# Kernel tuning notes

Hardware: AMD Instinct MI355X
Metric: run time of the kernel (lower is better)

The kernel has to match this reference:

```python
import jax, jax.numpy as jnp
import numpy as np

GS = 96  # grid_size per axis
NV, H_IM, W_IM = 8, 256, 256


def _world_grid():
    xs = jnp.linspace(-1.0, 1.0, GS)
    ys = jnp.linspace(-1.0, 1.0, GS)
    zs = jnp.linspace(0.0, 1.0, GS)
    gx, gy, gz = jnp.meshgrid(xs, ys, zs, indexing='ij')
    return jnp.stack([gx, gy, gz], -1).reshape(-1, 3)  # (N,3)


def _grid_sample(feats, grid):
    # feats (NV,C,H,W), grid (NV,P,2) normalized coords; bilinear,
    # align_corners=True, padding_mode='zeros' (matches F.grid_sample).
    n, C, H, W = feats.shape
    ix = (grid[..., 0] + 1.0) * (W - 1) * 0.5
    iy = (grid[..., 1] + 1.0) * (H - 1) * 0.5
    x0 = jnp.floor(ix); y0 = jnp.floor(iy)
    wx = (ix - x0)[..., None]; wy = (iy - y0)[..., None]
    x0i = x0.astype(jnp.int32); y0i = y0.astype(jnp.int32)
    b = jnp.arange(n)[:, None]
    def corner(yi, xi):
        valid = ((yi >= 0) & (yi < H) & (xi >= 0) & (xi < W)).astype(feats.dtype)
        v = feats[b, :, jnp.clip(yi, 0, H - 1), jnp.clip(xi, 0, W - 1)]  # (NV,P,C)
        return v * valid[..., None]
    v00 = corner(y0i, x0i); v01 = corner(y0i, x0i + 1)
    v10 = corner(y0i + 1, x0i); v11 = corner(y0i + 1, x0i + 1)
    return (v00 * (1 - wx) * (1 - wy) + v01 * wx * (1 - wy)
            + v10 * (1 - wx) * wy + v11 * wx * wy)


def _mlp_agg(x, w1, b1, w2, b2):
    h = jax.nn.relu(x @ w1.T + b1)
    return h @ w2.T + b2


def _forward(images, poses, focal, c, dw1, db1, dw2, db2, dw3, db3,
             ayz_w1, ayz_b1, ayz_w2, ayz_b2,
             axz_w1, axz_b1, axz_w2, axz_b2,
             axy_w1, axy_b1, axy_w2, axy_b2):
    nv, _, H, W = images.shape
    H_feat, W_feat = H // 2, W // 2
    stride = H / H_feat
    f = focal[0, 0] / stride
    f2 = jnp.stack([f, -f])                # y-focal flipped as in torch code
    c2 = c[0] / stride
    # features = unprocess_images(images): inverse of Normalize(0.5, 0.5)
    feats = images * 0.5 + 0.5             # (NV,3,H,W)

    wg = _world_grid()                     # (N,3)
    t = poses[:, :3, 3]; R = poses[:, :3, :3]
    d = wg[None] - t[:, None]              # (NV,N,3) dirs from cam center
    cam = jnp.einsum('npj,nji->npi', d, R) # world2camera: R^T (w - t)
    dnorm = jnp.linalg.norm(d + 1e-9, axis=-1)
    dirs = d / dnorm[..., None]

    uv = cam[..., :2] / cam[..., 2:3] * f2 + c2
    gxn = 2.0 * uv[..., 0] / (W_feat - 1) - 1.0
    gyn = 2.0 * uv[..., 1] / (H_feat - 1) - 1.0
    grid = jnp.stack([gxn, gyn], -1)       # (NV,N,2)
    mask_z = cam[..., 2] < 0.001
    inside = (jnp.abs(gxn) <= 1.0) & (jnp.abs(gyn) <= 1.0) & mask_z

    lat = _grid_sample(feats, grid) * inside[..., None].astype(images.dtype)  # (NV,N,3)
    out_latent = jnp.transpose(lat, (0, 2, 1))  # (NV,3,N)
    dirs = dirs * mask_z[..., None].astype(images.dtype)

    x = jnp.concatenate([lat, cam, dirs], -1)   # (NV,N,9)
    h = jax.nn.relu(x @ dw1.T + db1)
    h = jax.nn.relu(h @ dw2.T + db2)
    h = h @ dw3.T + db3                         # (NV,N,3)
    lat5 = h.reshape(1, nv, GS, GS, GS, 3)      # out_latent_2
    latm = lat5.mean(1)                         # (1,GS,GS,GS,3)

    coords = wg.reshape(1, GS, GS, GS, 3)
    w_yz = jax.nn.softmax(_mlp_agg(jnp.concatenate([latm, coords[..., 0:1]], -1), ayz_w1, ayz_b1, ayz_w2, ayz_b2), axis=1)
    w_xz = jax.nn.softmax(_mlp_agg(jnp.concatenate([latm, coords[..., 1:2]], -1), axz_w1, axz_b1, axz_w2, axz_b2), axis=2)
    w_xy = jax.nn.softmax(_mlp_agg(jnp.concatenate([latm, coords[..., 2:3]], -1), axy_w1, axy_b1, axy_w2, axy_b2), axis=3)

    fl_yz = (latm * w_yz).sum(1)   # (1,GS,GS,3)
    fl_xz = (latm * w_xz).sum(2)
    fl_xy = (latm * w_xy).sum(3)
    scene_xz = jnp.transpose(fl_xz, (0, 3, 1, 2))
    scene_xy = jnp.transpose(fl_xy, (0, 3, 1, 2))
    scene_yz = jnp.transpose(fl_yz, (0, 3, 1, 2))
    return scene_xz, scene_xy, scene_yz, out_latent, lat5


def _look_at(eye, target, up):
    f = target - eye; f = f / np.linalg.norm(f)
    z = -f
    x = np.cross(up, z); x = x / np.linalg.norm(x)
    y = np.cross(z, x)
    pose = np.eye(4, dtype=np.float32)
    pose[:3, 0] = x; pose[:3, 1] = y; pose[:3, 2] = z; pose[:3, 3] = eye
    return pose


def setup_inputs() -> dict:
    key = jax.random.key(0)
    ks = jax.random.split(key, 16)
    images = jax.random.normal(ks[0], (NV, 3, H_IM, W_IM), dtype=jnp.float32)
    # camera-to-world poses: ring of cameras looking at grid center (0,0,0.5)
    target = np.array([0.0, 0.0, 0.5], dtype=np.float32)
    up = np.array([0.0, 0.0, 1.0], dtype=np.float32)
    poses = np.stack([_look_at(np.array([3.0 * np.cos(a), 3.0 * np.sin(a), 1.5], dtype=np.float32), target, up)
                      for a in np.linspace(0, 2 * np.pi, NV, endpoint=False)])
    poses = jnp.asarray(poses)
    focal = jnp.full((1, 1), 300.0, dtype=jnp.float32)
    c = jnp.array([[W_IM / 2.0, H_IM / 2.0]], dtype=jnp.float32)

    def kaiming(k, shape):  # (out,in)
        return jax.random.normal(k, shape, dtype=jnp.float32) * np.sqrt(2.0 / shape[1])
    def bias(k, n):
        return jax.random.uniform(k, (n,), minval=-0.001, maxval=0.001, dtype=jnp.float32)

    inp = dict(images=images, poses=poses, focal=focal, c=c,
               dw1=kaiming(ks[1], (3, 9)), db1=bias(ks[2], 3),
               dw2=kaiming(ks[3], (3, 3)), db2=bias(ks[4], 3),
               dw3=kaiming(ks[5], (3, 3)), db3=bias(ks[6], 3),
               ayz_w1=kaiming(ks[7], (3, 4)), ayz_b1=bias(ks[8], 3),
               ayz_w2=kaiming(ks[9], (1, 3)), ayz_b2=bias(ks[10], 1),
               axz_w1=kaiming(ks[11], (3, 4)), axz_b1=bias(ks[12], 3),
               axz_w2=kaiming(ks[13], (1, 3)), axz_b2=bias(ks[14], 1),
               axy_w1=kaiming(ks[15], (3, 4)), axy_b1=bias(jax.random.fold_in(key, 99), 3),
               axy_w2=kaiming(jax.random.fold_in(key, 100), (1, 3)), axy_b2=bias(jax.random.fold_in(key, 101), 1))
    return inp


def reference(images, poses, focal, c, dw1, db1, dw2, db2, dw3, db3,
              ayz_w1, ayz_b1, ayz_w2, ayz_b2,
              axz_w1, axz_b1, axz_w2, axz_b2,
              axy_w1, axy_b1, axy_w2, axy_b2):
    return _forward(images, poses, focal, c, dw1, db1, dw2, db2, dw3, db3,
                    ayz_w1, ayz_b1, ayz_w2, ayz_b2,
                    axz_w1, axz_b1, axz_w2, axz_b2,
                    axy_w1, axy_b1, axy_w2, axy_b2)
```

## Files before the change

### kernel.cpp

```cpp
#include <hip/hip_runtime.h>
#include <math.h>

#define GSZ  96
#define GS2  (GSZ*GSZ)
#define NPTS (GSZ*GSZ*GSZ)
#define NVIEW 8
#define HIM  256
#define WIM  256

#define SCENE_SZ   (3*GS2)
#define OUTLAT_OFF (3*SCENE_SZ)
#define LAT5_OFF   (OUTLAT_OFF + NVIEW*3*NPTS)

__device__ __forceinline__ float red_max64(float v) {
    #pragma unroll
    for (int m = 32; m >= 1; m >>= 1) v = fmaxf(v, __shfl_xor(v, m, 64));
    return v;
}
__device__ __forceinline__ float red_sum64(float v) {
    #pragma unroll
    for (int m = 32; m >= 1; m >>= 1) v += __shfl_xor(v, m, 64);
    return v;
}

__global__ __launch_bounds__(256)
void k1_sample_mlp(const float* __restrict__ images, const float* __restrict__ poses,
                   const float* __restrict__ focal, const float* __restrict__ cc,
                   const float* __restrict__ dw1, const float* __restrict__ db1,
                   const float* __restrict__ dw2, const float* __restrict__ db2,
                   const float* __restrict__ dw3, const float* __restrict__ db3,
                   float* __restrict__ out_latent, float* __restrict__ lat5,
                   float* __restrict__ latm, int write_latm)
{
    const int p   = blockIdx.x * 256 + threadIdx.x;
    const int ix  = p / GS2;
    const int rem = p - ix * GS2;
    const int iy  = rem / GSZ;
    const int iz  = rem - iy * GSZ;
    const float wxv = (float)ix * (2.0f/95.0f) - 1.0f;
    const float wyv = (float)iy * (2.0f/95.0f) - 1.0f;
    const float wzv = (float)iz * (1.0f/95.0f);

    const float f   = focal[0] * 0.5f;
    const float c2x = cc[0] * 0.5f;
    const float c2y = cc[1] * 0.5f;

    float a0 = 0.f, a1 = 0.f, a2 = 0.f;

    for (int n = 0; n < NVIEW; ++n) {
        const float* ps = poses + n * 16;
        const float r00 = ps[0], r01 = ps[1], r02 = ps[2],  tx = ps[3];
        const float r10 = ps[4], r11 = ps[5], r12 = ps[6],  ty = ps[7];
        const float r20 = ps[8], r21 = ps[9], r22 = ps[10], tz = ps[11];

        const float dx = wxv - tx, dy = wyv - ty, dz = wzv - tz;
        const float camx = dx*r00 + dy*r10 + dz*r20;
        const float camy = dx*r01 + dy*r11 + dz*r21;
        const float camz = dx*r02 + dy*r12 + dz*r22;

        const float ex = dx + 1e-9f, ey = dy + 1e-9f, ez = dz + 1e-9f;
        const float dn = sqrtf(ex*ex + ey*ey + ez*ez);
        const bool  mz = camz < 0.001f;
        float d0 = 0.f, d1 = 0.f, d2 = 0.f;
        if (mz) { d0 = dx/dn; d1 = dy/dn; d2 = dz/dn; }

        const float u = camx/camz * f    + c2x;
        const float v = camy/camz * (-f) + c2y;
        const float gxn = 2.0f*u/127.0f - 1.0f;
        const float gyn = 2.0f*v/127.0f - 1.0f;

        float l0 = 0.f, l1 = 0.f, l2 = 0.f;
        const bool inside = (fabsf(gxn) <= 1.0f) && (fabsf(gyn) <= 1.0f) && mz;
        if (inside) {
            const float sx = (gxn + 1.0f) * 255.0f * 0.5f;
            const float sy = (gyn + 1.0f) * 255.0f * 0.5f;
            const float x0f = floorf(sx), y0f = floorf(sy);
            const float fx = sx - x0f, fy = sy - y0f;
            const int x0 = (int)x0f, y0 = (int)y0f;
            const int x1 = x0 + 1,  y1 = y0 + 1;
            const float vx0 = (x0 >= 0 && x0 < WIM) ? 1.f : 0.f;
            const float vx1 = (x1 >= 0 && x1 < WIM) ? 1.f : 0.f;
            const float vy0 = (y0 >= 0 && y0 < HIM) ? 1.f : 0.f;
            const float vy1 = (y1 >= 0 && y1 < HIM) ? 1.f : 0.f;
            const int cx0 = min(max(x0, 0), WIM-1), cx1 = min(max(x1, 0), WIM-1);
            const int cy0 = min(max(y0, 0), HIM-1), cy1 = min(max(y1, 0), HIM-1);
            const float w00 = (1.0f-fx)*(1.0f-fy)*vx0*vy0;
            const float w01 = fx*(1.0f-fy)*vx1*vy0;
            const float w10 = (1.0f-fx)*fy*vx0*vy1;
            const float w11 = fx*fy*vx1*vy1;
            const float* img = images + (size_t)n*3*HIM*WIM;
            #pragma unroll
            for (int ch = 0; ch < 3; ++ch) {
                const float* b = img + ch*HIM*WIM;
                const float p00 = b[cy0*WIM + cx0]*0.5f + 0.5f;
                const float p01 = b[cy0*WIM + cx1]*0.5f + 0.5f;
                const float p10 = b[cy1*WIM + cx0]*0.5f + 0.5f;
                const float p11 = b[cy1*WIM + cx1]*0.5f + 0.5f;
                const float lv  = p00*w00 + p01*w01 + p10*w10 + p11*w11;
                if (ch == 0) l0 = lv; else if (ch == 1) l1 = lv; else l2 = lv;
            }
        }

        __builtin_nontemporal_store(l0, out_latent + (size_t)n*3*NPTS + 0*NPTS + p);
        __builtin_nontemporal_store(l1, out_latent + (size_t)n*3*NPTS + 1*NPTS + p);
        __builtin_nontemporal_store(l2, out_latent + (size_t)n*3*NPTS + 2*NPTS + p);

        float xin[9] = {l0, l1, l2, camx, camy, camz, d0, d1, d2};
        float h1[3], h2[3], h3[3];
        #pragma unroll
        for (int k = 0; k < 3; ++k) {
            float s = 0.f;
            #pragma unroll
            for (int j = 0; j < 9; ++j) s += xin[j] * dw1[k*9 + j];
            s += db1[k];
            h1[k] = fmaxf(s, 0.f);
        }
        #pragma unroll
        for (int k = 0; k < 3; ++k) {
            float s = 0.f;
            #pragma unroll
            for (int j = 0; j < 3; ++j) s += h1[j] * dw2[k*3 + j];
            s += db2[k];
            h2[k] = fmaxf(s, 0.f);
        }
        #pragma unroll
        for (int k = 0; k < 3; ++k) {
            float s = 0.f;
            #pragma unroll
            for (int j = 0; j < 3; ++j) s += h2[j] * dw3[k*3 + j];
            s += db3[k];
            h3[k] = s;
        }

        float* lp = lat5 + ((size_t)n*NPTS + p)*3;
        __builtin_nontemporal_store(h3[0], lp + 0);
        __builtin_nontemporal_store(h3[1], lp + 1);
        __builtin_nontemporal_store(h3[2], lp + 2);
        a0 += h3[0]; a1 += h3[1]; a2 += h3[2];
    }

    if (write_latm) {
        latm[0*NPTS + p] = a0 * 0.125f;
        latm[1*NPTS + p] = a1 * 0.125f;
        latm[2*NPTS + p] = a2 * 0.125f;
    }
}

__global__ __launch_bounds__(64)
void k2_agg(const float* __restrict__ latm, const float* __restrict__ lat5, int use_ws,
            const float* __restrict__ yzw1, const float* __restrict__ yzb1,
            const float* __restrict__ yzw2, const float* __restrict__ yzb2,
            const float* __restrict__ xzw1, const float* __restrict__ xzb1,
            const float* __restrict__ xzw2, const float* __restrict__ xzb2,
            const float* __restrict__ xyw1, const float* __restrict__ xyb1,
            const float* __restrict__ xyw2, const float* __restrict__ xyb2,
            float* __restrict__ out)
{
    const int dir = blockIdx.y;
    const int l   = blockIdx.x;
    const int t   = threadIdx.x;
    const int la  = l / GSZ;
    const int lb  = l - la * GSZ;

    const float* w1 = (dir == 0) ? yzw1 : (dir == 1) ? xzw1 : xyw1;
    const float* b1 = (dir == 0) ? yzb1 : (dir == 1) ? xzb1 : xyb1;
    const float* w2 = (dir == 0) ? yzw2 : (dir == 1) ? xzw2 : xyw2;
    const float* b2 = (dir == 0) ? yzb2 : (dir == 1) ? xzb2 : xyb2;

    auto eval = [&](int vi, float& s, float& v0, float& v1, float& v2) {
        int p;
        float coord;
        if (dir == 0)      { p = vi*GS2 + la*GSZ + lb; coord = (float)vi*(2.0f/95.0f) - 1.0f; }
        else if (dir == 1) { p = la*GS2 + vi*GSZ + lb; coord = (float)vi*(2.0f/95.0f) - 1.0f; }
        else               { p = la*GS2 + lb*GSZ + vi; coord = (float)vi*(1.0f/95.0f); }
        if (use_ws) {
            v0 = latm[p]; v1 = latm[NPTS + p]; v2 = latm[2*NPTS + p];
        } else {
            v0 = 0.f; v1 = 0.f; v2 = 0.f;
            for (int n = 0; n < NVIEW; ++n) {
                const float* q = lat5 + ((size_t)n*NPTS + p)*3;
                v0 += q[0]; v1 += q[1]; v2 += q[2];
            }
            v0 *= 0.125f; v1 *= 0.125f; v2 *= 0.125f;
        }
        float h[3];
        #pragma unroll
        for (int k = 0; k < 3; ++k) {
            float a = v0*w1[k*4+0] + v1*w1[k*4+1] + v2*w1[k*4+2] + coord*w1[k*4+3] + b1[k];
            h[k] = fmaxf(a, 0.f);
        }
        s = h[0]*w2[0] + h[1]*w2[1] + h[2]*w2[2] + b2[0];
    };

    float s0, va0, va1, va2;
    eval(t, s0, va0, va1, va2);
    const bool hasB = (t < GSZ - 64);
    float s1 = -__builtin_inff(), vb0 = 0.f, vb1 = 0.f, vb2 = 0.f;
    if (hasB) eval(t + 64, s1, vb0, vb1, vb2);

    float m = red_max64(fmaxf(s0, s1));
    const float e0 = expf(s0 - m);
    const float e1 = hasB ? expf(s1 - m) : 0.f;

    float den = red_sum64(e0 + e1);
    float n0  = red_sum64(e0*va0 + e1*vb0);
    float n1  = red_sum64(e0*va1 + e1*vb1);
    float n2  = red_sum64(e0*va2 + e1*vb2);

    if (t == 0) {
        float* base = out + ((dir == 0) ? 2*SCENE_SZ : (dir == 1) ? 0 : SCENE_SZ);
        base[0*GS2 + la*GSZ + lb] = n0 / den;
        base[1*GS2 + la*GSZ + lb] = n1 / den;
        base[2*GS2 + la*GSZ + lb] = n2 / den;
    }
}

extern "C" void kernel_launch(void* const* d_in, const int* in_sizes, int n_in,
                              void* d_out, int out_size, void* d_ws, size_t ws_size,
                              hipStream_t stream) {
    const float* images = (const float*)d_in[0];
    const float* poses  = (const float*)d_in[1];
    const float* focal  = (const float*)d_in[2];
    const float* cc     = (const float*)d_in[3];
    const float* dw1 = (const float*)d_in[4];  const float* db1 = (const float*)d_in[5];
    const float* dw2 = (const float*)d_in[6];  const float* db2 = (const float*)d_in[7];
    const float* dw3 = (const float*)d_in[8];  const float* db3 = (const float*)d_in[9];
    const float* yzw1 = (const float*)d_in[10]; const float* yzb1 = (const float*)d_in[11];
    const float* yzw2 = (const float*)d_in[12]; const float* yzb2 = (const float*)d_in[13];
    const float* xzw1 = (const float*)d_in[14]; const float* xzb1 = (const float*)d_in[15];
    const float* xzw2 = (const float*)d_in[16]; const float* xzb2 = (const float*)d_in[17];
    const float* xyw1 = (const float*)d_in[18]; const float* xyb1 = (const float*)d_in[19];
    const float* xyw2 = (const float*)d_in[20]; const float* xyb2 = (const float*)d_in[21];

    float* out        = (float*)d_out;
    float* out_latent = out + OUTLAT_OFF;
    float* lat5       = out + LAT5_OFF;
    float* latm       = (float*)d_ws;
    const int use_ws  = (d_ws != nullptr &&
                         ws_size >= (size_t)NPTS * 3 * sizeof(float)) ? 1 : 0;

    hipLaunchKernelGGL(k1_sample_mlp, dim3(NPTS/256), dim3(256), 0, stream,
                       images, poses, focal, cc, dw1, db1, dw2, db2, dw3, db3,
                       out_latent, lat5, latm, use_ws);
    hipLaunchKernelGGL(k2_agg, dim3(GS2, 3), dim3(64), 0, stream,
                       latm, lat5, use_ws,
                       yzw1, yzb1, yzw2, yzb2,
                       xzw1, xzb1, xzw2, xzb2,
                       xyw1, xyb1, xyw2, xyb2,
                       out);
}
```

Measured before the change: 386.0 us.

## Interleave image channels, tile sampling in 2D, split aggregation into per-axis kernels

Adds a pre-pass that packs the three normalized image channels into float4 texels, so each bilinear corner becomes one vector load instead of three scattered loads. The sampling kernel now maps each block to a 16x16 y-z tile on one x slice, aiming for better locality of image gathers. Aggregation along x and y becomes one thread per line with an online softmax that reads coalesced across threads and keeps the weights in registers. Aggregation along z keeps the wave reduction but packs four lines per block. The cost is an extra kernel launch and an 8 MB workspace buffer for the packed images.

Result: faster. 308.8 us (-20.0%).

```diff
diff --git a/kernel.cpp b/kernel.cpp
--- a/kernel.cpp
+++ b/kernel.cpp
@@ -7,10 +7,14 @@
 #define NVIEW 8
 #define HIM  256
 #define WIM  256
+#define NPIX (HIM*WIM)
 
 #define SCENE_SZ   (3*GS2)
 #define OUTLAT_OFF (3*SCENE_SZ)
 #define LAT5_OFF   (OUTLAT_OFF + NVIEW*3*NPTS)
+
+#define LATM_BYTES ((size_t)3*NPTS*sizeof(float))
+#define IMG4_BYTES ((size_t)NVIEW*NPIX*sizeof(float4))
 
 __device__ __forceinline__ float red_max64(float v) {
     #pragma unroll
@@ -24,7 +28,24 @@
 }
 
 __global__ __launch_bounds__(256)
-void k1_sample_mlp(const float* __restrict__ images, const float* __restrict__ poses,
+void k0_interleave(const float* __restrict__ images, float4* __restrict__ img4)
+{
+    const int g   = blockIdx.x * 256 + threadIdx.x;
+    const int n   = g >> 16;
+    const int pix = g & (NPIX - 1);
+    const float* base = images + (size_t)n * 3 * NPIX + pix;
+    float4 v;
+    v.x = base[0]        * 0.5f + 0.5f;
+    v.y = base[NPIX]     * 0.5f + 0.5f;
+    v.z = base[2*NPIX]   * 0.5f + 0.5f;
+    v.w = 0.f;
+    img4[g] = v;
+}
+
+__global__ __launch_bounds__(256)
+void k1_sample_mlp(const float* __restrict__ images, const float4* __restrict__ img4,
+                   int use_img4,
+                   const float* __restrict__ poses,
                    const float* __restrict__ focal, const float* __restrict__ cc,
                    const float* __restrict__ dw1, const float* __restrict__ db1,
                    const float* __restrict__ dw2, const float* __restrict__ db2,
@@ -32,11 +53,13 @@
                    float* __restrict__ out_latent, float* __restrict__ lat5,
                    float* __restrict__ latm, int write_latm)
 {
-    const int p   = blockIdx.x * 256 + threadIdx.x;
-    const int ix  = p / GS2;
-    const int rem = p - ix * GS2;
-    const int iy  = rem / GSZ;
-    const int iz  = rem - iy * GSZ;
+    const int ty = threadIdx.x >> 4;
+    const int tz = threadIdx.x & 15;
+    const int iy = blockIdx.x * 16 + ty;
+    const int iz = blockIdx.y * 16 + tz;
+    const int ix = blockIdx.z;
+    const int p  = ix * GS2 + iy * GSZ + iz;
+
     const float wxv = (float)ix * (2.0f/95.0f) - 1.0f;
     const float wyv = (float)iy * (2.0f/95.0f) - 1.0f;
     const float wzv = (float)iz * (1.0f/95.0f);
@@ -50,10 +73,10 @@
     for (int n = 0; n < NVIEW; ++n) {
         const float* ps = poses + n * 16;
         const float r00 = ps[0], r01 = ps[1], r02 = ps[2],  tx = ps[3];
-        const float r10 = ps[4], r11 = ps[5], r12 = ps[6],  ty = ps[7];
-        const float r20 = ps[8], r21 = ps[9], r22 = ps[10], tz = ps[11];
-
-        const float dx = wxv - tx, dy = wyv - ty, dz = wzv - tz;
+        const float r10 = ps[4], r11 = ps[5], r12 = ps[6],  tyy = ps[7];
+        const float r20 = ps[8], r21 = ps[9], r22 = ps[10], tzz = ps[11];
+
+        const float dx = wxv - tx, dy = wyv - tyy, dz = wzv - tzz;
         const float camx = dx*r00 + dy*r10 + dz*r20;
         const float camy = dx*r01 + dy*r11 + dz*r21;
         const float camz = dx*r02 + dy*r12 + dz*r22;
@@ -88,16 +111,27 @@
             const float w01 = fx*(1.0f-fy)*vx1*vy0;
             const float w10 = (1.0f-fx)*fy*vx0*vy1;
             const float w11 = fx*fy*vx1*vy1;
-            const float* img = images + (size_t)n*3*HIM*WIM;
-            #pragma unroll
-            for (int ch = 0; ch < 3; ++ch) {
-                const float* b = img + ch*HIM*WIM;
-                const float p00 = b[cy0*WIM + cx0]*0.5f + 0.5f;
-                const float p01 = b[cy0*WIM + cx1]*0.5f + 0.5f;
-                const float p10 = b[cy1*WIM + cx0]*0.5f + 0.5f;
-                const float p11 = b[cy1*WIM + cx1]*0.5f + 0.5f;
-                const float lv  = p00*w00 + p01*w01 + p10*w10 + p11*w11;
-                if (ch == 0) l0 = lv; else if (ch == 1) l1 = lv; else l2 = lv;
+            if (use_img4) {
+                const float4* iv = img4 + (size_t)n * NPIX;
+                const float4 q00 = iv[cy0*WIM + cx0];
+                const float4 q01 = iv[cy0*WIM + cx1];
+                const float4 q10 = iv[cy1*WIM + cx0];
+                const float4 q11 = iv[cy1*WIM + cx1];
+                l0 = q00.x*w00 + q01.x*w01 + q10.x*w10 + q11.x*w11;
+                l1 = q00.y*w00 + q01.y*w01 + q10.y*w10 + q11.y*w11;
+                l2 = q00.z*w00 + q01.z*w01 + q10.z*w10 + q11.z*w11;
+            } else {
+                const float* img = images + (size_t)n*3*NPIX;
+                #pragma unroll
+                for (int ch = 0; ch < 3; ++ch) {
+                    const float* b = img + ch*NPIX;
+                    const float p00 = b[cy0*WIM + cx0]*0.5f + 0.5f;
+                    const float p01 = b[cy0*WIM + cx1]*0.5f + 0.5f;
+                    const float p10 = b[cy1*WIM + cx0]*0.5f + 0.5f;
+                    const float p11 = b[cy1*WIM + cx1]*0.5f + 0.5f;
+                    const float lv  = p00*w00 + p01*w01 + p10*w10 + p11*w11;
+                    if (ch == 0) l0 = lv; else if (ch == 1) l1 = lv; else l2 = lv;
+                }
             }
         }
 
@@ -112,24 +146,21 @@
             float s = 0.f;
             #pragma unroll
             for (int j = 0; j < 9; ++j) s += xin[j] * dw1[k*9 + j];
-            s += db1[k];
-            h1[k] = fmaxf(s, 0.f);
+            h1[k] = fmaxf(s + db1[k], 0.f);
         }
         #pragma unroll
         for (int k = 0; k < 3; ++k) {
             float s = 0.f;
             #pragma unroll
             for (int j = 0; j < 3; ++j) s += h1[j] * dw2[k*3 + j];
-            s += db2[k];
-            h2[k] = fmaxf(s, 0.f);
+            h2[k] = fmaxf(s + db2[k], 0.f);
         }
         #pragma unroll
         for (int k = 0; k < 3; ++k) {
             float s = 0.f;
             #pragma unroll
             for (int j = 0; j < 3; ++j) s += h2[j] * dw3[k*3 + j];
-            s += db3[k];
-            h3[k] = s;
+            h3[k] = s + db3[k];
         }
 
         float* lp = lat5 + ((size_t)n*NPTS + p)*3;
@@ -146,33 +177,35 @@
     }
 }
 
-__global__ __launch_bounds__(64)
-void k2_agg(const float* __restrict__ latm, const float* __restrict__ lat5, int use_ws,
-            const float* __restrict__ yzw1, const float* __restrict__ yzb1,
-            const float* __restrict__ yzw2, const float* __restrict__ yzb2,
-            const float* __restrict__ xzw1, const float* __restrict__ xzb1,
-            const float* __restrict__ xzw2, const float* __restrict__ xzb2,
-            const float* __restrict__ xyw1, const float* __restrict__ xyb1,
-            const float* __restrict__ xyw2, const float* __restrict__ xyb2,
-            float* __restrict__ out)
+__global__ __launch_bounds__(256)
+void k2a_lines(const float* __restrict__ latm, const float* __restrict__ lat5, int use_ws,
+               const float* __restrict__ yzw1, const float* __restrict__ yzb1,
+               const float* __restrict__ yzw2, const float* __restrict__ yzb2,
+               const float* __restrict__ xzw1, const float* __restrict__ xzb1,
+               const float* __restrict__ xzw2, const float* __restrict__ xzb2,
+               float* __restrict__ out)
 {
     const int dir = blockIdx.y;
-    const int l   = blockIdx.x;
-    const int t   = threadIdx.x;
-    const int la  = l / GSZ;
-    const int lb  = l - la * GSZ;
-
-    const float* w1 = (dir == 0) ? yzw1 : (dir == 1) ? xzw1 : xyw1;
-    const float* b1 = (dir == 0) ? yzb1 : (dir == 1) ? xzb1 : xyb1;
-    const float* w2 = (dir == 0) ? yzw2 : (dir == 1) ? xzw2 : xyw2;
-    const float* b2 = (dir == 0) ? yzb2 : (dir == 1) ? xzb2 : xyb2;
-
-    auto eval = [&](int vi, float& s, float& v0, float& v1, float& v2) {
-        int p;
-        float coord;
-        if (dir == 0)      { p = vi*GS2 + la*GSZ + lb; coord = (float)vi*(2.0f/95.0f) - 1.0f; }
-        else if (dir == 1) { p = la*GS2 + vi*GSZ + lb; coord = (float)vi*(2.0f/95.0f) - 1.0f; }
-        else               { p = la*GS2 + lb*GSZ + vi; coord = (float)vi*(1.0f/95.0f); }
+    const int t   = blockIdx.x * 256 + threadIdx.x;
+    const int la  = t / GSZ;
+    const int lb  = t - la * GSZ;
+
+    const float* w1 = (dir == 0) ? yzw1 : xzw1;
+    const float* b1 = (dir == 0) ? yzb1 : xzb1;
+    const float* w2 = (dir == 0) ? yzw2 : xzw2;
+    const float* b2 = (dir == 0) ? yzb2 : xzb2;
+    float W1[12], B1[3], W2[3];
+    #pragma unroll
+    for (int k = 0; k < 12; ++k) W1[k] = w1[k];
+    #pragma unroll
+    for (int k = 0; k < 3;  ++k) { B1[k] = b1[k]; W2[k] = w2[k]; }
+    const float B2 = b2[0];
+
+    float m = -INFINITY, den = 0.f, q0 = 0.f, q1 = 0.f, q2 = 0.f;
+    for (int vi = 0; vi < GSZ; ++vi) {
+        const int p = (dir == 0) ? (vi*GS2 + t) : (la*GS2 + vi*GSZ + lb);
+        const float coord = (float)vi * (2.0f/95.0f) - 1.0f;
+        float v0, v1, v2;
         if (use_ws) {
             v0 = latm[p]; v1 = latm[NPTS + p]; v2 = latm[2*NPTS + p];
         } else {
@@ -186,29 +219,76 @@
         float h[3];
         #pragma unroll
         for (int k = 0; k < 3; ++k) {
-            float a = v0*w1[k*4+0] + v1*w1[k*4+1] + v2*w1[k*4+2] + coord*w1[k*4+3] + b1[k];
+            float a = v0*W1[k*4+0] + v1*W1[k*4+1] + v2*W1[k*4+2] + coord*W1[k*4+3] + B1[k];
             h[k] = fmaxf(a, 0.f);
         }
-        s = h[0]*w2[0] + h[1]*w2[1] + h[2]*w2[2] + b2[0];
+        const float s = h[0]*W2[0] + h[1]*W2[1] + h[2]*W2[2] + B2;
+        const float mn = fmaxf(m, s);
+        const float c  = expf(m - mn);
+        const float e  = expf(s - mn);
+        den = den*c + e;
+        q0  = q0*c + e*v0;
+        q1  = q1*c + e*v1;
+        q2  = q2*c + e*v2;
+        m = mn;
+    }
+    float* base = out + ((dir == 0) ? 2*SCENE_SZ : 0);
+    base[0*GS2 + t] = q0 / den;
+    base[1*GS2 + t] = q1 / den;
+    base[2*GS2 + t] = q2 / den;
+}
+
+__global__ __launch_bounds__(256)
+void k2b_zlines(const float* __restrict__ latm, const float* __restrict__ lat5, int use_ws,
+                const float* __restrict__ xyw1, const float* __restrict__ xyb1,
+                const float* __restrict__ xyw2, const float* __restrict__ xyb2,
+                float* __restrict__ out)
+{
+    const int wv = threadIdx.x >> 6;
+    const int t  = threadIdx.x & 63;
+    const int l  = blockIdx.x * 4 + wv;
+    const int la = l / GSZ;
+    const int lb = l - la * GSZ;
+
+    auto eval = [&](int vi, float& s, float& v0, float& v1, float& v2) {
+        const int p = la*GS2 + lb*GSZ + vi;
+        const float coord = (float)vi * (1.0f/95.0f);
+        if (use_ws) {
+            v0 = latm[p]; v1 = latm[NPTS + p]; v2 = latm[2*NPTS + p];
+        } else {
+            v0 = 0.f; v1 = 0.f; v2 = 0.f;
+            for (int n = 0; n < NVIEW; ++n) {
+                const float* q = lat5 + ((size_t)n*NPTS + p)*3;
+                v0 += q[0]; v1 += q[1]; v2 += q[2];
+            }
+            v0 *= 0.125f; v1 *= 0.125f; v2 *= 0.125f;
+        }
+        float h[3];
+        #pragma unroll
+        for (int k = 0; k < 3; ++k) {
+            float a = v0*xyw1[k*4+0] + v1*xyw1[k*4+1] + v2*xyw1[k*4+2] + coord*xyw1[k*4+3] + xyb1[k];
+            h[k] = fmaxf(a, 0.f);
+        }
+        s = h[0]*xyw2[0] + h[1]*xyw2[1] + h[2]*xyw2[2] + xyb2[0];
     };
 
     float s0, va0, va1, va2;
     eval(t, s0, va0, va1, va2);
     const bool hasB = (t < GSZ - 64);
-    float s1 = -__builtin_inff(), vb0 = 0.f, vb1 = 0.f, vb2 = 0.f;
+    float s1 = -INFINITY, vb0 = 0.f, vb1 = 0.f, vb2 = 0.f;
     if (hasB) eval(t + 64, s1, vb0, vb1, vb2);
 
-    float m = red_max64(fmaxf(s0, s1));
+    const float m  = red_max64(fmaxf(s0, s1));
     const float e0 = expf(s0 - m);
     const float e1 = hasB ? expf(s1 - m) : 0.f;
 
-    float den = red_sum64(e0 + e1);
-    float n0  = red_sum64(e0*va0 + e1*vb0);
-    float n1  = red_sum64(e0*va1 + e1*vb1);
-    float n2  = red_sum64(e0*va2 + e1*vb2);
+    const float den = red_sum64(e0 + e1);
+    const float n0  = red_sum64(e0*va0 + e1*vb0);
+    const float n1  = red_sum64(e0*va1 + e1*vb1);
+    const float n2  = red_sum64(e0*va2 + e1*vb2);
 
     if (t == 0) {
-        float* base = out + ((dir == 0) ? 2*SCENE_SZ : (dir == 1) ? 0 : SCENE_SZ);
+        float* base = out + SCENE_SZ;
         base[0*GS2 + la*GSZ + lb] = n0 / den;
         base[1*GS2 + la*GSZ + lb] = n1 / den;
         base[2*GS2 + la*GSZ + lb] = n2 / den;
@@ -236,16 +316,26 @@
     float* out_latent = out + OUTLAT_OFF;
     float* lat5       = out + LAT5_OFF;
     float* latm       = (float*)d_ws;
-    const int use_ws  = (d_ws != nullptr &&
-                         ws_size >= (size_t)NPTS * 3 * sizeof(float)) ? 1 : 0;
-
-    hipLaunchKernelGGL(k1_sample_mlp, dim3(NPTS/256), dim3(256), 0, stream,
-                       images, poses, focal, cc, dw1, db1, dw2, db2, dw3, db3,
+    float4* img4      = (float4*)((char*)d_ws + LATM_BYTES);
+
+    const int use_ws   = (d_ws != nullptr && ws_size >= LATM_BYTES) ? 1 : 0;
+    const int use_img4 = (d_ws != nullptr && ws_size >= LATM_BYTES + IMG4_BYTES) ? 1 : 0;
+
+    if (use_img4) {
+        hipLaunchKernelGGL(k0_interleave, dim3(NVIEW*NPIX/256), dim3(256), 0, stream,
+                           images, img4);
+    }
+    hipLaunchKernelGGL(k1_sample_mlp, dim3(6, 6, 96), dim3(256), 0, stream,
+                       images, img4, use_img4, poses, focal, cc,
+                       dw1, db1, dw2, db2, dw3, db3,
                        out_latent, lat5, latm, use_ws);
-    hipLaunchKernelGGL(k2_agg, dim3(GS2, 3), dim3(64), 0, stream,
+    hipLaunchKernelGGL(k2a_lines, dim3(GS2/256, 2), dim3(256), 0, stream,
                        latm, lat5, use_ws,
                        yzw1, yzb1, yzw2, yzb2,
                        xzw1, xzb1, xzw2, xzb2,
+                       out);
+    hipLaunchKernelGGL(k2b_zlines, dim3(GS2/4), dim3(256), 0, stream,
+                       latm, lat5, use_ws,
                        xyw1, xyb1, xyw2, xyb2,
                        out);
 }
```
